# Optimization experiments

Measured on AMD Instinct MI355X. Metric: run time of the kernel, lower is better.

Reference implementation:

```python
import jax, jax.numpy as jnp
import numpy as np

D = 512        # d_model == pretrain_dim
V = 8192       # vocab_size
B, T, U = 2, 256, 64


def setup_inputs() -> dict:
    key = jax.random.key(0)
    ks = jax.random.split(key, 8)
    s = 1.0 / np.sqrt(D)
    return {
        "v":  jax.random.normal(ks[0], (B, T, D), jnp.float32),
        "t":  jax.random.normal(ks[1], (B, U, D), jnp.float32),
        "W1": jax.random.normal(ks[2], (D, D), jnp.float32) * s,
        "b1": jax.random.normal(ks[3], (D,), jnp.float32) * s,
        "W2": jax.random.normal(ks[4], (D, D), jnp.float32) * s,
        "b2": jax.random.normal(ks[5], (D,), jnp.float32) * s,
        "Wv": jax.random.normal(ks[6], (D, V), jnp.float32) * s,
        "bv": jax.random.normal(ks[7], (V,), jnp.float32) * s,
    }


def reference(v, t, W1, b1, W2, b2, Wv, bv):
    # fc1 / fc2 are pointwise linears, so applying them BEFORE the broadcast
    # is mathematically identical to the original repeat-then-linear code,
    # but avoids redundantly projecting each frame/token T*U times.
    enc = jnp.einsum('btd,de->bte', v, W1) + b1           # (B,T,D)
    dec = jnp.einsum('bud,de->bue', t, W2) + b2           # (B,U,D)
    h = jax.nn.relu(enc[:, :, None, :] + dec[:, None, :, :])  # (B,T,U,D)
    logits = jnp.einsum('btud,dv->btuv', h, Wv) + bv      # (B,T,U,V)
    return jax.nn.log_softmax(logits, axis=-1)
```

## Files before the change

### kernel.cpp

```cpp
#include <hip/hip_runtime.h>
#include <hip/hip_bf16.h>
#include <stdint.h>

#define D_ 512
#define V_ 8192
#define B_ 2
#define T_ 256
#define U_ 64
#define M_ (B_*T_*U_)
#define BT_ (B_*T_)
#define BU_ (B_*U_)

typedef __bf16 bf16x8 __attribute__((ext_vector_type(8)));
typedef float  floatx4 __attribute__((ext_vector_type(4)));

__device__ inline void load16_lds(const void* g, void* l) {
  __builtin_amdgcn_global_load_lds(
      (const __attribute__((address_space(1))) uint32_t*)(uintptr_t)g,
      (__attribute__((address_space(3))) uint32_t*)(uintptr_t)l,
      16, 0, 0);
}

__global__ __launch_bounds__(256) void encdec_kernel(
    const float* __restrict__ v, const float* __restrict__ t,
    const float* __restrict__ W1, const float* __restrict__ b1,
    const float* __restrict__ W2, const float* __restrict__ b2,
    float* __restrict__ enc, float* __restrict__ dec) {
  __shared__ float xs[D_];
  int r = blockIdx.x;
  const float* x; const float* W; const float* bias; float* out;
  if (r < BT_) { x = v + (size_t)r*D_;          W = W1; bias = b1; out = enc + (size_t)r*D_; }
  else         { int rr = r - BT_;
                 x = t + (size_t)rr*D_;         W = W2; bias = b2; out = dec + (size_t)rr*D_; }
  int tid = threadIdx.x;
  xs[tid]       = x[tid];
  xs[tid + 256] = x[tid + 256];
  __syncthreads();
  float a0 = 0.f, a1 = 0.f;
  int c0 = tid * 2;
  #pragma unroll 8
  for (int k = 0; k < D_; ++k) {
    float xv = xs[k];
    float2 w = *(const float2*)(W + (size_t)k*D_ + c0);
    a0 += xv * w.x;
    a1 += xv * w.y;
  }
  float2 o; o.x = a0 + bias[c0]; o.y = a1 + bias[c0+1];
  *(float2*)(out + c0) = o;
}

__global__ __launch_bounds__(256) void wv_transpose_kernel(
    const float* __restrict__ Wv, __bf16* __restrict__ WvT) {
  __shared__ float tile[64][65];
  int k0 = (blockIdx.x & 7) * 64;
  int n0 = (blockIdx.x >> 3) * 64;
  int tid = threadIdx.x;
  int c  = tid & 63;
  int r0 = tid >> 6;
  #pragma unroll
  for (int i = 0; i < 64; i += 4)
    tile[r0 + i][c] = Wv[(size_t)(k0 + r0 + i) * V_ + n0 + c];
  __syncthreads();
  #pragma unroll
  for (int i = 0; i < 64; i += 4)
    WvT[(size_t)(n0 + r0 + i) * D_ + k0 + c] = (__bf16)tile[c][r0 + i];
}

__global__ __launch_bounds__(256) void build_h_kernel(
    const float* __restrict__ enc, const float* __restrict__ dec,
    __bf16* __restrict__ h) {
  int tid = blockIdx.x * 256 + threadIdx.x;
  int m  = tid >> 6;
  int kc = (tid & 63) << 3;
  int bt = m >> 6;
  int dr = ((m >> 14) << 6) | (m & 63);
  const float4* e4 = (const float4*)(enc + (size_t)bt*D_ + kc);
  const float4* d4 = (const float4*)(dec + (size_t)dr*D_ + kc);
  float4 e0 = e4[0], e1 = e4[1];
  float4 d0 = d4[0], d1 = d4[1];
  bf16x8 o;
  o[0] = (__bf16)fmaxf(e0.x + d0.x, 0.f);
  o[1] = (__bf16)fmaxf(e0.y + d0.y, 0.f);
  o[2] = (__bf16)fmaxf(e0.z + d0.z, 0.f);
  o[3] = (__bf16)fmaxf(e0.w + d0.w, 0.f);
  o[4] = (__bf16)fmaxf(e1.x + d1.x, 0.f);
  o[5] = (__bf16)fmaxf(e1.y + d1.y, 0.f);
  o[6] = (__bf16)fmaxf(e1.z + d1.z, 0.f);
  o[7] = (__bf16)fmaxf(e1.w + d1.w, 0.f);
  *(bf16x8*)(h + (size_t)m*D_ + kc) = o;
}

#define BM 128
#define BN 128
#define BKk 64

__global__ __launch_bounds__(256) void gemm_kernel(
    const __bf16* __restrict__ h, const __bf16* __restrict__ WvT,
    const float* __restrict__ bv, float* __restrict__ out,
    float* __restrict__ lse) {
  __shared__ __bf16 As[BM * BKk];
  __shared__ __bf16 Bs[BN * BKk];
  const int tid  = threadIdx.x;
  const int lane = tid & 63;
  const int w    = tid >> 6;
  const int wm   = w & 1, wn = w >> 1;
  const int bid  = blockIdx.x;
  const int gm0  = (bid & 255) * BM;
  const int gn0  = (bid >> 8) * BN;
  const int quad = lane >> 4;
  const int l15  = lane & 15;
  const int key  = lane & 7;

  floatx4 acc[4][4];
  #pragma unroll
  for (int a = 0; a < 4; ++a)
    #pragma unroll
    for (int b = 0; b < 4; ++b)
      acc[a][b] = (floatx4){0.f, 0.f, 0.f, 0.f};

  for (int ki = 0; ki < D_/BKk; ++ki) {
    const int k0 = ki * BKk;
    #pragma unroll
    for (int i = 0; i < 4; ++i) {
      int s = i * 256 + tid;
      int r = s >> 3;
      int c = (s & 7) ^ (r & 7);
      load16_lds(h   + (size_t)(gm0 + r)*D_ + k0 + c*8, As + s*8);
      load16_lds(WvT + (size_t)(gn0 + r)*D_ + k0 + c*8, Bs + s*8);
    }
    __syncthreads();
    #pragma unroll
    for (int kk = 0; kk < 2; ++kk) {
      bf16x8 af[4], bfr[4];
      const int cslot = (kk*4 + quad) ^ key;
      #pragma unroll
      for (int mt = 0; mt < 4; ++mt) {
        int r = wm*64 + mt*16 + l15;
        af[mt] = *(const bf16x8*)(As + (r*8 + cslot)*8);
      }
      #pragma unroll
      for (int nt = 0; nt < 4; ++nt) {
        int r = wn*64 + nt*16 + l15;
        bfr[nt] = *(const bf16x8*)(Bs + (r*8 + cslot)*8);
      }
      #pragma unroll
      for (int mt = 0; mt < 4; ++mt)
        #pragma unroll
        for (int nt = 0; nt < 4; ++nt)
          acc[mt][nt] = __builtin_amdgcn_mfma_f32_16x16x32_bf16(
              af[mt], bfr[nt], acc[mt][nt], 0, 0, 0);
    }
    __syncthreads();
  }

  float bvv[4];
  #pragma unroll
  for (int nt = 0; nt < 4; ++nt)
    bvv[nt] = bv[gn0 + wn*64 + nt*16 + l15];

  #pragma unroll
  for (int mt = 0; mt < 4; ++mt) {
    const int rg = gm0 + wm*64 + mt*16 + quad*4;
    #pragma unroll
    for (int i = 0; i < 4; ++i) {
      float s = 0.f;
      #pragma unroll
      for (int nt = 0; nt < 4; ++nt) {
        float lg = acc[mt][nt][i] + bvv[nt];
        out[(size_t)(rg + i)*V_ + gn0 + wn*64 + nt*16 + l15] = lg;
        s += exp2f(lg * 1.44269504088896f);
      }
      #pragma unroll
      for (int off = 1; off < 16; off <<= 1)
        s += __shfl_xor(s, off, 64);
      if (l15 == 0) atomicAdd(&lse[rg + i], s);
    }
  }
}

__global__ __launch_bounds__(256) void lse_log_kernel(float* lse) {
  int i = blockIdx.x * 256 + threadIdx.x;
  lse[i] = logf(lse[i]);
}

__global__ __launch_bounds__(256) void subtract_kernel(
    float4* __restrict__ out4, const float* __restrict__ lse) {
  const long long n4 = (long long)M_ * V_ / 4;
  long long i = (long long)blockIdx.x * 256 + threadIdx.x;
  const long long stride = (long long)gridDim.x * 256;
  for (; i < n4; i += stride) {
    int row = (int)(i >> 11);
    float l = lse[row];
    float4 vv = out4[i];
    vv.x -= l; vv.y -= l; vv.z -= l; vv.w -= l;
    out4[i] = vv;
  }
}

extern "C" void kernel_launch(void* const* d_in, const int* in_sizes, int n_in,
                              void* d_out, int out_size, void* d_ws, size_t ws_size,
                              hipStream_t stream) {
  const float* v  = (const float*)d_in[0];
  const float* t  = (const float*)d_in[1];
  const float* W1 = (const float*)d_in[2];
  const float* b1 = (const float*)d_in[3];
  const float* W2 = (const float*)d_in[4];
  const float* b2 = (const float*)d_in[5];
  const float* Wv = (const float*)d_in[6];
  const float* bv = (const float*)d_in[7];
  float* out = (float*)d_out;

  char* ws = (char*)d_ws;
  float*  enc = (float*)(ws);
  float*  dec = (float*)(ws + (1u<<20));
  float*  lse = (float*)(ws + (1u<<20) + (256u<<10));
  __bf16* WvT = (__bf16*)(ws + (2u<<20));
  __bf16* h   = (__bf16*)(ws + (10u<<20));

  hipMemsetAsync(lse, 0, M_*sizeof(float), stream);
  encdec_kernel<<<BT_ + BU_, 256, 0, stream>>>(v, t, W1, b1, W2, b2, enc, dec);
  wv_transpose_kernel<<<1024, 256, 0, stream>>>(Wv, WvT);
  build_h_kernel<<<(M_*D_/8)/256, 256, 0, stream>>>(enc, dec, h);
  gemm_kernel<<<(M_/BM)*(V_/BN), 256, 0, stream>>>(h, WvT, bv, out, lse);
  lse_log_kernel<<<M_/256, 256, 0, stream>>>(lse);
  subtract_kernel<<<8192, 256, 0, stream>>>((float4*)out, lse);
}
```

Measured before the change: 1.959 ms.

## Fuse GEMM and log-softmax into a two-pass recompute kernel per row block

```diff
diff --git a/kernel.cpp b/kernel.cpp
--- a/kernel.cpp
+++ b/kernel.cpp
@@ -93,107 +93,171 @@
 #define BM 128
 #define BN 128
 #define BKk 64
-
-__global__ __launch_bounds__(256) void gemm_kernel(
+#define NTILES (V_/BN)
+#define QTOT   (NTILES*(D_/BKk))
+
+__global__ __launch_bounds__(512) void fused_lsm_kernel(
     const __bf16* __restrict__ h, const __bf16* __restrict__ WvT,
-    const float* __restrict__ bv, float* __restrict__ out,
-    float* __restrict__ lse) {
-  __shared__ __bf16 As[BM * BKk];
-  __shared__ __bf16 Bs[BN * BKk];
+    const float* __restrict__ bv, float* __restrict__ out) {
+  __shared__ __bf16 As[BM * D_];
+  __shared__ __bf16 Bs[2][BN * BKk];
+
   const int tid  = threadIdx.x;
   const int lane = tid & 63;
   const int w    = tid >> 6;
-  const int wm   = w & 1, wn = w >> 1;
-  const int bid  = blockIdx.x;
-  const int gm0  = (bid & 255) * BM;
-  const int gn0  = (bid >> 8) * BN;
+  const int wm   = w & 1;
+  const int wn   = w >> 1;
   const int quad = lane >> 4;
   const int l15  = lane & 15;
   const int key  = lane & 7;
-
-  floatx4 acc[4][4];
-  #pragma unroll
-  for (int a = 0; a < 4; ++a)
+  const int gm0  = blockIdx.x * BM;
+
+  #pragma unroll
+  for (int it = 0; it < 16; ++it) {
+    int s  = it * 512 + tid;
+    int r  = s >> 6;
+    int sc = s & 63;
+    int c  = (sc & ~7) | ((sc & 7) ^ (r & 7));
+    load16_lds(h + (size_t)(gm0 + r) * D_ + c * 8, As + (size_t)s * 8);
+  }
+  #pragma unroll
+  for (int it = 0; it < 2; ++it) {
+    int s = it * 512 + tid;
+    int r = s >> 3;
+    int c = (s & 7) ^ (r & 7);
+    load16_lds(WvT + (size_t)r * D_ + c * 8, Bs[0] + s * 8);
+  }
+  asm volatile("s_waitcnt vmcnt(0)" ::: "memory");
+  __builtin_amdgcn_s_barrier();
+  asm volatile("" ::: "memory");
+
+  float sacc[4][4];
+  #pragma unroll
+  for (int mt = 0; mt < 4; ++mt)
     #pragma unroll
-    for (int b = 0; b < 4; ++b)
-      acc[a][b] = (floatx4){0.f, 0.f, 0.f, 0.f};
-
-  for (int ki = 0; ki < D_/BKk; ++ki) {
-    const int k0 = ki * BKk;
-    #pragma unroll
-    for (int i = 0; i < 4; ++i) {
-      int s = i * 256 + tid;
-      int r = s >> 3;
-      int c = (s & 7) ^ (r & 7);
-      load16_lds(h   + (size_t)(gm0 + r)*D_ + k0 + c*8, As + s*8);
-      load16_lds(WvT + (size_t)(gn0 + r)*D_ + k0 + c*8, Bs + s*8);
+    for (int i = 0; i < 4; ++i) sacc[mt][i] = 0.f;
+  float lseR[4][4];
+
+  for (int pass = 0; pass < 2; ++pass) {
+    for (int n = 0; n < NTILES; ++n) {
+      floatx4 acc[4][2];
+      #pragma unroll
+      for (int mt = 0; mt < 4; ++mt)
+        #pragma unroll
+        for (int nt = 0; nt < 2; ++nt)
+          acc[mt][nt] = (floatx4){0.f, 0.f, 0.f, 0.f};
+
+      for (int ki = 0; ki < 8; ++ki) {
+        const int q   = n * 8 + ki;
+        const int cur = q & 1;
+        if (!(pass == 1 && q == QTOT - 1)) {
+          const int qq = (q + 1) & (QTOT - 1);
+          const int nn = qq >> 3, kn = qq & 7;
+          #pragma unroll
+          for (int it = 0; it < 2; ++it) {
+            int s = it * 512 + tid;
+            int r = s >> 3;
+            int c = (s & 7) ^ (r & 7);
+            load16_lds(WvT + (size_t)(nn * BN + r) * D_ + kn * BKk + c * 8,
+                       Bs[cur ^ 1] + s * 8);
+          }
+          asm volatile("s_waitcnt vmcnt(2)" ::: "memory");
+        } else {
+          asm volatile("s_waitcnt vmcnt(0)" ::: "memory");
+        }
+        __builtin_amdgcn_s_barrier();
+        asm volatile("" ::: "memory");
+
+        const __bf16* bcur = &Bs[cur][0];
+        #pragma unroll
+        for (int kk = 0; kk < 2; ++kk) {
+          bf16x8 af[4], bfr[2];
+          const int cA = ki * 8 + kk * 4 + quad;
+          const int sA = (cA & ~7) | ((cA & 7) ^ key);
+          #pragma unroll
+          for (int mt = 0; mt < 4; ++mt) {
+            int r = wm * 64 + mt * 16 + l15;
+            af[mt] = *(const bf16x8*)(As + (size_t)(r * 64 + sA) * 8);
+          }
+          const int sB = (kk * 4 + quad) ^ key;
+          #pragma unroll
+          for (int nt = 0; nt < 2; ++nt) {
+            int r = wn * 32 + nt * 16 + l15;
+            bfr[nt] = *(const bf16x8*)(bcur + (size_t)(r * 8 + sB) * 8);
+          }
+          #pragma unroll
+          for (int mt = 0; mt < 4; ++mt)
+            #pragma unroll
+            for (int nt = 0; nt < 2; ++nt)
+              acc[mt][nt] = __builtin_amdgcn_mfma_f32_16x16x32_bf16(
+                  af[mt], bfr[nt], acc[mt][nt], 0, 0, 0);
+        }
+        asm volatile("" ::: "memory");
+        __builtin_amdgcn_s_barrier();
+      }
+
+      float bvv[2];
+      #pragma unroll
+      for (int nt = 0; nt < 2; ++nt)
+        bvv[nt] = bv[n * BN + wn * 32 + nt * 16 + l15];
+
+      if (pass == 0) {
+        #pragma unroll
+        for (int mt = 0; mt < 4; ++mt)
+          #pragma unroll
+          for (int i = 0; i < 4; ++i) {
+            float s = sacc[mt][i];
+            #pragma unroll
+            for (int nt = 0; nt < 2; ++nt)
+              s += exp2f((acc[mt][nt][i] + bvv[nt]) * 1.44269504088896f);
+            sacc[mt][i] = s;
+          }
+      } else {
+        #pragma unroll
+        for (int mt = 0; mt < 4; ++mt)
+          #pragma unroll
+          for (int i = 0; i < 4; ++i) {
+            const int row = gm0 + wm * 64 + mt * 16 + quad * 4 + i;
+            const float l = lseR[mt][i];
+            #pragma unroll
+            for (int nt = 0; nt < 2; ++nt)
+              out[(size_t)row * V_ + n * BN + wn * 32 + nt * 16 + l15] =
+                  acc[mt][nt][i] + bvv[nt] - l;
+          }
+      }
     }
-    __syncthreads();
-    #pragma unroll
-    for (int kk = 0; kk < 2; ++kk) {
-      bf16x8 af[4], bfr[4];
-      const int cslot = (kk*4 + quad) ^ key;
-      #pragma unroll
-      for (int mt = 0; mt < 4; ++mt) {
-        int r = wm*64 + mt*16 + l15;
-        af[mt] = *(const bf16x8*)(As + (r*8 + cslot)*8);
+
+    if (pass == 0) {
+      #pragma unroll
+      for (int mt = 0; mt < 4; ++mt)
+        #pragma unroll
+        for (int i = 0; i < 4; ++i) {
+          float s = sacc[mt][i];
+          s += __shfl_xor(s, 1, 64);
+          s += __shfl_xor(s, 2, 64);
+          s += __shfl_xor(s, 4, 64);
+          s += __shfl_xor(s, 8, 64);
+          sacc[mt][i] = s;
+        }
+      __syncthreads();
+      float* scr = (float*)&Bs[1][0];
+      if (l15 == 0) {
+        #pragma unroll
+        for (int mt = 0; mt < 4; ++mt)
+          #pragma unroll
+          for (int i = 0; i < 4; ++i)
+            scr[wn * 128 + wm * 64 + mt * 16 + quad * 4 + i] = sacc[mt][i];
       }
-      #pragma unroll
-      for (int nt = 0; nt < 4; ++nt) {
-        int r = wn*64 + nt*16 + l15;
-        bfr[nt] = *(const bf16x8*)(Bs + (r*8 + cslot)*8);
-      }
+      __syncthreads();
       #pragma unroll
       for (int mt = 0; mt < 4; ++mt)
         #pragma unroll
-        for (int nt = 0; nt < 4; ++nt)
-          acc[mt][nt] = __builtin_amdgcn_mfma_f32_16x16x32_bf16(
-              af[mt], bfr[nt], acc[mt][nt], 0, 0, 0);
+        for (int i = 0; i < 4; ++i) {
+          int r = wm * 64 + mt * 16 + quad * 4 + i;
+          lseR[mt][i] = logf(scr[r] + scr[128 + r] + scr[256 + r] + scr[384 + r]);
+        }
+      __syncthreads();
     }
-    __syncthreads();
-  }
-
-  float bvv[4];
-  #pragma unroll
-  for (int nt = 0; nt < 4; ++nt)
-    bvv[nt] = bv[gn0 + wn*64 + nt*16 + l15];
-
-  #pragma unroll
-  for (int mt = 0; mt < 4; ++mt) {
-    const int rg = gm0 + wm*64 + mt*16 + quad*4;
-    #pragma unroll
-    for (int i = 0; i < 4; ++i) {
-      float s = 0.f;
-      #pragma unroll
-      for (int nt = 0; nt < 4; ++nt) {
-        float lg = acc[mt][nt][i] + bvv[nt];
-        out[(size_t)(rg + i)*V_ + gn0 + wn*64 + nt*16 + l15] = lg;
-        s += exp2f(lg * 1.44269504088896f);
-      }
-      #pragma unroll
-      for (int off = 1; off < 16; off <<= 1)
-        s += __shfl_xor(s, off, 64);
-      if (l15 == 0) atomicAdd(&lse[rg + i], s);
-    }
-  }
-}
-
-__global__ __launch_bounds__(256) void lse_log_kernel(float* lse) {
-  int i = blockIdx.x * 256 + threadIdx.x;
-  lse[i] = logf(lse[i]);
-}
-
-__global__ __launch_bounds__(256) void subtract_kernel(
-    float4* __restrict__ out4, const float* __restrict__ lse) {
-  const long long n4 = (long long)M_ * V_ / 4;
-  long long i = (long long)blockIdx.x * 256 + threadIdx.x;
-  const long long stride = (long long)gridDim.x * 256;
-  for (; i < n4; i += stride) {
-    int row = (int)(i >> 11);
-    float l = lse[row];
-    float4 vv = out4[i];
-    vv.x -= l; vv.y -= l; vv.z -= l; vv.w -= l;
-    out4[i] = vv;
   }
 }
 
@@ -213,15 +277,11 @@
   char* ws = (char*)d_ws;
   float*  enc = (float*)(ws);
   float*  dec = (float*)(ws + (1u<<20));
-  float*  lse = (float*)(ws + (1u<<20) + (256u<<10));
   __bf16* WvT = (__bf16*)(ws + (2u<<20));
   __bf16* h   = (__bf16*)(ws + (10u<<20));
 
-  hipMemsetAsync(lse, 0, M_*sizeof(float), stream);
   encdec_kernel<<<BT_ + BU_, 256, 0, stream>>>(v, t, W1, b1, W2, b2, enc, dec);
   wv_transpose_kernel<<<1024, 256, 0, stream>>>(Wv, WvT);
   build_h_kernel<<<(M_*D_/8)/256, 256, 0, stream>>>(enc, dec, h);
-  gemm_kernel<<<(M_/BM)*(V_/BN), 256, 0, stream>>>(h, WvT, bv, out, lse);
-  lse_log_kernel<<<M_/256, 256, 0, stream>>>(lse);
-  subtract_kernel<<<8192, 256, 0, stream>>>((float4*)out, lse);
-}
+  fused_lsm_kernel<<<M_/BM, 512, 0, stream>>>(h, WvT, bv, out);
+}
```

New measurement: 1.776 ms. -9.4%, faster.
